# Kernel optimization log

Hardware: AMD Instinct MI355X
Metric: run time of the kernel (lower is better)

Reference implementation:

```python
import jax, jax.numpy as jnp
import numpy as np

N = 100_000   # nodes
E = 1_600_000 # edges
F = 128       # featurenum
H = 32        # hidden size (hard-coded in module)
G = 256       # graphs in batch


def setup_inputs() -> dict:
    key = jax.random.key(0)
    ks = jax.random.split(key, 10)
    x = jax.random.normal(ks[0], (N, F), jnp.float32)
    edge_index = jax.random.randint(ks[1], (2, E), 0, N)
    edge_attr = jax.random.randint(ks[2], (E, 1), 0, 4)
    batch = jnp.sort(jax.random.randint(ks[3], (N,), 0, G))
    def w(k, shape, fan):
        return jax.random.normal(k, shape, jnp.float32) / np.float32(np.sqrt(fan))
    W1 = w(ks[4], (F, H), F); b1 = jnp.zeros((H,), jnp.float32)
    W2 = w(ks[5], (H, H), H); b2 = jnp.zeros((H,), jnp.float32)
    Wl = w(ks[6], (H, 4 * H), H); bl = jnp.zeros((4 * H,), jnp.float32)
    Wm1 = w(ks[7], (H, H), H); bm1 = jnp.zeros((H,), jnp.float32)
    Wm2 = w(ks[8], (H, 1), H); bm2 = jnp.zeros((1,), jnp.float32)
    return dict(x=x, edge_index=edge_index, edge_attr=edge_attr, batch=batch,
                W1=W1, b1=b1, W2=W2, b2=b2, Wl=Wl, bl=bl,
                Wm1=Wm1, bm1=bm1, Wm2=Wm2, bm2=bm2)


def gcn_conv(x, src, tgt, W, b, n):
    # PyG GCNConv: add self-loops, symmetric normalization D^-1/2 (A+I) D^-1/2
    xw = x @ W                                            # [n, out]
    ones = jnp.ones(tgt.shape[0], x.dtype)
    deg = jax.ops.segment_sum(ones, tgt, num_segments=n) + 1.0  # in-degree + self-loop
    dinv = jax.lax.rsqrt(deg)
    msg = (dinv[src] * dinv[tgt])[:, None] * xw[src]      # [E, out]
    out = jax.ops.segment_sum(msg, tgt, num_segments=n)
    out = out + xw * (1.0 / deg)[:, None]                 # self-loop term (norm = 1/deg)
    return out + b


def reference(x, edge_index, edge_attr, batch, W1, b1, W2, b2, Wl, bl, Wm1, bm1, Wm2, bm2):
    n = x.shape[0]
    src, tgt = edge_index[0], edge_index[1]
    h = jax.nn.relu(gcn_conv(x, src, tgt, W1, b1, n))
    h = jax.nn.relu(gcn_conv(h, src, tgt, W2, b2, n))
    # MPNNl: linear -> (n, 4, H), gather slot per edge, scatter-mean to targets
    hl = (h @ Wl + bl).reshape(n, 4, H)
    rs = hl[src, edge_attr[:, 0]]                         # [E, H]
    cnt = jax.ops.segment_sum(jnp.ones(tgt.shape[0], h.dtype), tgt, num_segments=n)
    agg = jax.ops.segment_sum(rs, tgt, num_segments=n) / jnp.maximum(cnt, 1.0)[:, None]
    # global mean pool over graphs
    gcnt = jax.ops.segment_sum(jnp.ones(n, h.dtype), batch, num_segments=G)
    g = jax.ops.segment_sum(agg, batch, num_segments=G) / jnp.maximum(gcnt, 1.0)[:, None]
    # dropout in eval mode = identity; MLP + sigmoid
    out = jax.nn.relu(g @ Wm1 + bm1) @ Wm2 + bm2
    return jax.nn.sigmoid(out)                            # [G, 1]
```

## Files before the change

kernel.cpp:

```cpp
#include <hip/hip_runtime.h>
#include <hip/hip_bf16.h>
#include <stdint.h>

#define CDIV(a, b) (((a) + (b) - 1) / (b))

constexpr int BSH = 9;
#define TILE_A 2048

__global__ __launch_bounds__(256) void coarse_hist_k(const int* __restrict__ tgt,
                                                     int* __restrict__ bcnt, int E, int nb) {
    __shared__ int h[512];
    int t = threadIdx.x;
    for (int i = t; i < nb; i += 256) h[i] = 0;
    __syncthreads();
    for (int e = blockIdx.x * 256 + t; e < E; e += gridDim.x * 256)
        atomicAdd(&h[tgt[e] >> BSH], 1);
    __syncthreads();
    for (int i = t; i < nb; i += 256)
        if (h[i]) atomicAdd(&bcnt[i], h[i]);
}

__global__ __launch_bounds__(256) void bucket_scan_k(const int* __restrict__ bcnt,
                                                     int* __restrict__ bbase,
                                                     int* __restrict__ bcur, int nb, int E) {
    __shared__ int sp[256];
    int t = threadIdx.x;
    int c0 = (2 * t < nb) ? bcnt[2 * t] : 0;
    int c1 = (2 * t + 1 < nb) ? bcnt[2 * t + 1] : 0;
    int s2 = c0 + c1;
    sp[t] = s2;
    __syncthreads();
    for (int off = 1; off < 256; off <<= 1) {
        int x = (t >= off) ? sp[t - off] : 0;
        __syncthreads();
        sp[t] += x;
        __syncthreads();
    }
    int excl = sp[t] - s2;
    if (2 * t < nb) { bbase[2 * t] = excl; bcur[2 * t] = excl; }
    if (2 * t + 1 < nb) { bbase[2 * t + 1] = excl + c0; bcur[2 * t + 1] = excl + c0; }
    if (t == 0) bbase[nb] = E;
}

__global__ __launch_bounds__(256) void binA_k(const int* __restrict__ ei,
                                              const int* __restrict__ ea,
                                              int* __restrict__ bcur,
                                              unsigned long long* __restrict__ tmp, int E) {
    __shared__ unsigned long long stage[TILE_A];
    __shared__ int h_cnt[512], h_excl[512], h_cur[512], h_run[512], sp[256];
    int t = threadIdx.x;
    int base = blockIdx.x * TILE_A;
    int nt = min(TILE_A, E - base);
    for (int i = t; i < 512; i += 256) { h_cnt[i] = 0; h_cur[i] = 0; }
    __syncthreads();
    unsigned long long pk[8];
    int bk[8];
#pragma unroll
    for (int k = 0; k < 8; ++k) {
        int e = base + t + k * 256;
        bk[k] = -1;
        if (e < E) {
            int s = ei[e], tg = ei[E + e];
            unsigned a = (unsigned)ea[e];
            pk[k] = ((unsigned long long)(unsigned)tg << 20) |
                    ((unsigned long long)a << 18) | (unsigned long long)(unsigned)s;
            bk[k] = tg >> BSH;
            atomicAdd(&h_cnt[bk[k]], 1);
        }
    }
    __syncthreads();
    int c0 = h_cnt[2 * t], c1 = h_cnt[2 * t + 1];
    int s2 = c0 + c1;
    sp[t] = s2;
    __syncthreads();
    for (int off = 1; off < 256; off <<= 1) {
        int x = (t >= off) ? sp[t - off] : 0;
        __syncthreads();
        sp[t] += x;
        __syncthreads();
    }
    int excl = sp[t] - s2;
    h_excl[2 * t] = excl;
    h_excl[2 * t + 1] = excl + c0;
    __syncthreads();
    for (int i = t; i < 512; i += 256)
        if (h_cnt[i]) h_run[i] = atomicAdd(&bcur[i], h_cnt[i]);
#pragma unroll
    for (int k = 0; k < 8; ++k) {
        if (bk[k] >= 0) {
            int r = atomicAdd(&h_cur[bk[k]], 1);
            stage[h_excl[bk[k]] + r] = pk[k];
        }
    }
    __syncthreads();
    for (int i = t; i < nt; i += 256) {
        unsigned long long v = stage[i];
        int b = (int)(v >> 20) >> BSH;
        tmp[h_run[b] + (i - h_excl[b])] = v;
    }
}

__global__ __launch_bounds__(256) void binB_k(const unsigned long long* __restrict__ tmp,
                                              const int* __restrict__ bbase,
                                              unsigned* __restrict__ adj,
                                              int* __restrict__ rowptr4,
                                              float* __restrict__ dinv, int N, int E) {
    __shared__ int ncnt4[2048], nbase4[2048], ncur4[2048], sp[256];
    int t = threadIdx.x, b = blockIdx.x;
    int e0 = bbase[b], e1 = bbase[b + 1];
    int node0 = b << BSH;
    int nn = min(512, N - node0);
    for (int i = t; i < 2048; i += 256) { ncnt4[i] = 0; ncur4[i] = 0; }
    __syncthreads();
    for (int e = e0 + t; e < e1; e += 256) {
        unsigned long long v = tmp[e];
        int li = (int)(v >> 20) - node0;
        int q = (int)(v >> 18) & 3;
        atomicAdd(&ncnt4[li * 4 + q], 1);
    }
    __syncthreads();
    int loc[8];
    int s = 0;
#pragma unroll
    for (int k = 0; k < 8; ++k) { loc[k] = ncnt4[t * 8 + k]; s += loc[k]; }
    sp[t] = s;
    __syncthreads();
    for (int off = 1; off < 256; off <<= 1) {
        int x = (t >= off) ? sp[t - off] : 0;
        __syncthreads();
        sp[t] += x;
        __syncthreads();
    }
    int run = sp[t] - s;
#pragma unroll
    for (int k = 0; k < 8; ++k) { nbase4[t * 8 + k] = run; run += loc[k]; }
    __syncthreads();
    for (int i = t; i < nn; i += 256) {
        int node = node0 + i;
        *(int4*)&rowptr4[node * 4] = make_int4(e0 + nbase4[i * 4], e0 + nbase4[i * 4 + 1],
                                               e0 + nbase4[i * 4 + 2], e0 + nbase4[i * 4 + 3]);
        int c = ncnt4[i * 4] + ncnt4[i * 4 + 1] + ncnt4[i * 4 + 2] + ncnt4[i * 4 + 3];
        dinv[node] = rsqrtf((float)c + 1.0f);
    }
    if (b == 0 && t == 0) rowptr4[N * 4] = E;
    for (int e = e0 + t; e < e1; e += 256) {
        unsigned long long v = tmp[e];
        int li = (int)(v >> 20) - node0;
        int q = (int)(v >> 18) & 3;
        int r = atomicAdd(&ncur4[li * 4 + q], 1);
        adj[e0 + nbase4[li * 4 + q] + r] = (unsigned)(v & 0xFFFFFull);
    }
}

__device__ __forceinline__ int lb_sorted(const int* __restrict__ b, int n, int g) {
    int lo = 0, hi = n;
    while (lo < hi) {
        int m = (lo + hi) >> 1;
        if (b[m] < g) lo = m + 1; else hi = m;
    }
    return lo;
}

__global__ __launch_bounds__(256) void gbounds_k(const int* __restrict__ batch,
                                                 int* __restrict__ gcnt, int n, int Gn) {
    int g = blockIdx.x * 256 + threadIdx.x;
    if (g < Gn) {
        int a = lb_sorted(batch, n, g);
        int b2 = lb_sorted(batch, n, g + 1);
        gcnt[g] = b2 - a;
    }
}

__device__ __forceinline__ ushort f2bf(float v) {
    __hip_bfloat16 b = __float2bfloat16(v);
    return *reinterpret_cast<ushort*>(&b);
}
__device__ __forceinline__ float bflo(unsigned u) { return __uint_as_float(u << 16); }
__device__ __forceinline__ float bfhi(unsigned u) { return __uint_as_float(u & 0xFFFF0000u); }

template <int K, int COUT, int R, typename OutT>
__global__ __launch_bounds__(256) void gemm_rk(const float* __restrict__ X,
                                               const float* __restrict__ W,
                                               const float* __restrict__ bias,
                                               const float* __restrict__ dinv,
                                               OutT* __restrict__ Y, int nrows) {
    constexpr int NCG = COUT / 8;
    constexpr int RG = 256 / NCG;
    constexpr int ROWS = RG * R;
    constexpr int WS = K + 5;
    __shared__ float wt[COUT][WS];
    int t = threadIdx.x;
    for (int i = t; i < K * COUT; i += 256) {
        int k = i / COUT, j = i % COUT;
        wt[j][k] = W[i];
    }
    __syncthreads();
    int cg = t % NCG, g = t / NCG;
    int j0 = cg * 8;
    long rowbase = (long)blockIdx.x * ROWS + (long)g * R;
    float acc[R][8];
#pragma unroll
    for (int r = 0; r < R; ++r)
#pragma unroll
        for (int j = 0; j < 8; ++j) acc[r][j] = 0.0f;

    long rr[R];
#pragma unroll
    for (int r = 0; r < R; ++r) {
        long q = rowbase + r;
        rr[r] = (q < nrows) ? q : (long)(nrows - 1);
    }
    for (int k0 = 0; k0 < K; k0 += 4) {
        float4 xv[R];
#pragma unroll
        for (int r = 0; r < R; ++r) xv[r] = *(const float4*)(X + rr[r] * K + k0);
        float4 wv[8];
#pragma unroll
        for (int j = 0; j < 8; ++j) wv[j] = *(const float4*)&wt[j0 + j][k0];
#pragma unroll
        for (int r = 0; r < R; ++r)
#pragma unroll
            for (int j = 0; j < 8; ++j) {
                acc[r][j] += xv[r].x * wv[j].x;
                acc[r][j] += xv[r].y * wv[j].y;
                acc[r][j] += xv[r].z * wv[j].z;
                acc[r][j] += xv[r].w * wv[j].w;
            }
    }
#pragma unroll
    for (int r = 0; r < R; ++r) {
        long row = rowbase + r;
        if (row < nrows) {
            float dv = dinv ? dinv[row] : 1.0f;
            float o[8];
#pragma unroll
            for (int j = 0; j < 8; ++j) {
                float v = acc[r][j];
                if (bias) v += bias[j0 + j];
                o[j] = v * dv;
            }
            if constexpr (sizeof(OutT) == 4) {
                float4 o0 = make_float4(o[0], o[1], o[2], o[3]);
                float4 o1 = make_float4(o[4], o[5], o[6], o[7]);
                *(float4*)&Y[row * COUT + j0] = o0;
                *(float4*)&Y[row * COUT + j0 + 4] = o1;
            } else {
                uint4 u;
                u.x = (unsigned)f2bf(o[0]) | ((unsigned)f2bf(o[1]) << 16);
                u.y = (unsigned)f2bf(o[2]) | ((unsigned)f2bf(o[3]) << 16);
                u.z = (unsigned)f2bf(o[4]) | ((unsigned)f2bf(o[5]) << 16);
                u.w = (unsigned)f2bf(o[6]) | ((unsigned)f2bf(o[7]) << 16);
                *(uint4*)&Y[row * COUT + j0] = u;
            }
        }
    }
}


template <typename OutT>
__global__ __launch_bounds__(256) void agg_conv_k(const uint2* __restrict__ xwd4,
                                                  const unsigned* __restrict__ adj,
                                                  const int* __restrict__ rowptr4,
                                                  const float* __restrict__ dinv,
                                                  const float* __restrict__ bias,
                                                  OutT* __restrict__ out, int n) {
    int t = threadIdx.x;
    int node = blockIdx.x * 32 + (t >> 3);
    int f4 = t & 7;
    if (node >= n) return;
    int e0 = rowptr4[node * 4];
    int e1 = rowptr4[node * 4 + 4];
    float a0 = 0.f, a1 = 0.f, a2 = 0.f, a3 = 0.f;
    for (int e = e0; e < e1; e += 4) {
        int end1 = e1 - 1;
        int i1 = min(e + 1, end1), i2 = min(e + 2, end1), i3 = min(e + 3, end1);
        unsigned s0 = adj[e] & 0x3FFFF, s1 = adj[i1] & 0x3FFFF;
        unsigned s2 = adj[i2] & 0x3FFFF, s3 = adj[i3] & 0x3FFFF;
        uint2 u0 = xwd4[s0 * 8 + f4];
        uint2 u1 = xwd4[s1 * 8 + f4];
        uint2 u2 = xwd4[s2 * 8 + f4];
        uint2 u3 = xwd4[s3 * 8 + f4];
        bool v1 = e + 1 < e1, v2 = e + 2 < e1, v3 = e + 3 < e1;
        u1.x = v1 ? u1.x : 0u; u1.y = v1 ? u1.y : 0u;
        u2.x = v2 ? u2.x : 0u; u2.y = v2 ? u2.y : 0u;
        u3.x = v3 ? u3.x : 0u; u3.y = v3 ? u3.y : 0u;
        a0 += (bflo(u0.x) + bflo(u1.x)) + (bflo(u2.x) + bflo(u3.x));
        a1 += (bfhi(u0.x) + bfhi(u1.x)) + (bfhi(u2.x) + bfhi(u3.x));
        a2 += (bflo(u0.y) + bflo(u1.y)) + (bflo(u2.y) + bflo(u3.y));
        a3 += (bfhi(u0.y) + bfhi(u1.y)) + (bfhi(u2.y) + bfhi(u3.y));
    }
    float dvn = dinv[node];
    float degv = (float)(e1 - e0) + 1.0f;
    float sself = 1.0f / (dvn * degv);
    uint2 un = xwd4[node * 8 + f4];
    int c0i = 4 * f4;
    float v0 = fmaxf(dvn * a0 + bflo(un.x) * sself + bias[c0i], 0.0f);
    float v1 = fmaxf(dvn * a1 + bfhi(un.x) * sself + bias[c0i + 1], 0.0f);
    float v2 = fmaxf(dvn * a2 + bflo(un.y) * sself + bias[c0i + 2], 0.0f);
    float v3 = fmaxf(dvn * a3 + bfhi(un.y) * sself + bias[c0i + 3], 0.0f);
    if constexpr (sizeof(OutT) == 4) {
        *(float4*)&out[node * 32 + c0i] = make_float4(v0, v1, v2, v3);
    } else {
        uint2 w;
        w.x = (unsigned)f2bf(v0) | ((unsigned)f2bf(v1) << 16);
        w.y = (unsigned)f2bf(v2) | ((unsigned)f2bf(v3) << 16);
        ((uint2*)out)[node * 8 + f4] = w;
    }
}

#define RUN_ACC4(START, END, A)                                             \
    for (int e = (START); e < (END); e += 4) {                              \
        int end1 = (END) - 1;                                               \
        int i1 = min(e + 1, end1), i2 = min(e + 2, end1), i3 = min(e + 3, end1); \
        unsigned s0 = adj[e] & 0x3FFFF, s1 = adj[i1] & 0x3FFFF;             \
        unsigned s2 = adj[i2] & 0x3FFFF, s3 = adj[i3] & 0x3FFFF;            \
        uint2 u0 = h2q[s0 * 8 + f4];                                        \
        uint2 u1 = h2q[s1 * 8 + f4];                                        \
        uint2 u2 = h2q[s2 * 8 + f4];                                        \
        uint2 u3 = h2q[s3 * 8 + f4];                                        \
        bool v1 = e + 1 < (END), v2 = e + 2 < (END), v3 = e + 3 < (END);    \
        u1.x = v1 ? u1.x : 0u; u1.y = v1 ? u1.y : 0u;                       \
        u2.x = v2 ? u2.x : 0u; u2.y = v2 ? u2.y : 0u;                       \
        u3.x = v3 ? u3.x : 0u; u3.y = v3 ? u3.y : 0u;                       \
        (A).x += (bflo(u0.x) + bflo(u1.x)) + (bflo(u2.x) + bflo(u3.x));     \
        (A).y += (bfhi(u0.x) + bfhi(u1.x)) + (bfhi(u2.x) + bfhi(u3.x));     \
        (A).z += (bflo(u0.y) + bflo(u1.y)) + (bflo(u2.y) + bflo(u3.y));     \
        (A).w += (bfhi(u0.y) + bfhi(u1.y)) + (bfhi(u2.y) + bfhi(u3.y));     \
    }

__global__ __launch_bounds__(256) void agg_rs_fused_k(const uint2* __restrict__ h2q,
                                                      const unsigned* __restrict__ adj,
                                                      const int* __restrict__ rowptr4,
                                                      const float* __restrict__ Wl,
                                                      const float* __restrict__ bl,
                                                      float* __restrict__ out, int n) {
    constexpr int AS = 132;
    __shared__ float wls[32][128];
    __shared__ float bls[128];
    __shared__ float accs[32][AS];
    int t = threadIdx.x;
    for (int i = t; i < 4096; i += 256) wls[i >> 7][i & 127] = Wl[i];
    if (t < 128) bls[t] = bl[t];
    __syncthreads();

    int nl = t >> 3;
    int f4 = t & 7;
    int c0i = 4 * f4;
    int node = blockIdx.x * 32 + nl;
    if (node >= n) return;
    int4 rp = *(const int4*)&rowptr4[node * 4];
    int e4 = rowptr4[node * 4 + 4];
    float4 a0 = make_float4(0.f, 0.f, 0.f, 0.f);
    float4 a1 = a0, a2 = a0, a3 = a0;
    RUN_ACC4(rp.x, rp.y, a0)
    RUN_ACC4(rp.y, rp.z, a1)
    RUN_ACC4(rp.z, rp.w, a2)
    RUN_ACC4(rp.w, e4, a3)

    accs[nl][c0i] = a0.x;      accs[nl][c0i + 1] = a0.y;
    accs[nl][c0i + 2] = a0.z;  accs[nl][c0i + 3] = a0.w;
    accs[nl][32 + c0i] = a1.x;     accs[nl][32 + c0i + 1] = a1.y;
    accs[nl][32 + c0i + 2] = a1.z; accs[nl][32 + c0i + 3] = a1.w;
    accs[nl][64 + c0i] = a2.x;     accs[nl][64 + c0i + 1] = a2.y;
    accs[nl][64 + c0i + 2] = a2.z; accs[nl][64 + c0i + 3] = a2.w;
    accs[nl][96 + c0i] = a3.x;     accs[nl][96 + c0i + 1] = a3.y;
    accs[nl][96 + c0i + 2] = a3.z; accs[nl][96 + c0i + 3] = a3.w;
    float m0 = (float)(rp.y - rp.x), m1 = (float)(rp.z - rp.y);
    float m2 = (float)(rp.w - rp.z), m3 = (float)(e4 - rp.w);
    float o0 = m0 * bls[c0i] + m1 * bls[32 + c0i] + m2 * bls[64 + c0i] + m3 * bls[96 + c0i];
    float o1 = m0 * bls[c0i + 1] + m1 * bls[32 + c0i + 1] + m2 * bls[64 + c0i + 1] + m3 * bls[96 + c0i + 1];
    float o2 = m0 * bls[c0i + 2] + m1 * bls[32 + c0i + 2] + m2 * bls[64 + c0i + 2] + m3 * bls[96 + c0i + 2];
    float o3 = m0 * bls[c0i + 3] + m1 * bls[32 + c0i + 3] + m2 * bls[64 + c0i + 3] + m3 * bls[96 + c0i + 3];
#pragma unroll 8
    for (int j = 0; j < 32; ++j) {
        float q0 = accs[nl][j], q1 = accs[nl][32 + j];
        float q2 = accs[nl][64 + j], q3 = accs[nl][96 + j];
        float4 w0 = *(const float4*)&wls[j][c0i];
        float4 w1 = *(const float4*)&wls[j][32 + c0i];
        float4 w2 = *(const float4*)&wls[j][64 + c0i];
        float4 w3 = *(const float4*)&wls[j][96 + c0i];
        o0 += q0 * w0.x + q1 * w1.x + q2 * w2.x + q3 * w3.x;
        o1 += q0 * w0.y + q1 * w1.y + q2 * w2.y + q3 * w3.y;
        o2 += q0 * w0.z + q1 * w1.z + q2 * w2.z + q3 * w3.z;
        o3 += q0 * w0.w + q1 * w1.w + q2 * w2.w + q3 * w3.w;
    }
    float c = fmaxf((float)(e4 - rp.x), 1.0f);
    float ic = 1.0f / c;
    *(float4*)&out[node * 32 + c0i] = make_float4(o0 * ic, o1 * ic, o2 * ic, o3 * ic);
}


__global__ __launch_bounds__(256) void graph_sum_k(const float* __restrict__ agg,
                                                   const int* __restrict__ batch,
                                                   float* __restrict__ gsum, int n) {
    const int CHUNK = 128;
    int t = threadIdx.x;
    int f = t & 31;
    int j = t >> 5;
    long base = (long)blockIdx.x * (8 * CHUNK) + (long)j * CHUNK;
    if (base >= n) return;
    int end = (int)((n - base < CHUNK) ? (n - base) : CHUNK);
    int cur = batch[base];
    float acc = 0.0f;
    for (int i = 0; i < end; ++i) {
        int b = batch[base + i];
        if (b != cur) {
            atomicAdd(&gsum[cur * 32 + f], acc);
            acc = 0.0f;
            cur = b;
        }
        acc += agg[(base + i) * 32 + f];
    }
    atomicAdd(&gsum[cur * 32 + f], acc);
}


__global__ __launch_bounds__(256) void mlp_k(const float* __restrict__ gsum,
                                             const int* __restrict__ gcnt,
                                             const float* __restrict__ Wm1,
                                             const float* __restrict__ bm1,
                                             const float* __restrict__ Wm2,
                                             const float* __restrict__ bm2,
                                             float* __restrict__ out, int Gn) {
    __shared__ float w1[1024];
    __shared__ float w2[32];
    __shared__ float b1s[32];
    int t = threadIdx.x;
    for (int i = t; i < 1024; i += 256) w1[i] = Wm1[i];
    if (t < 32) {
        w2[t] = Wm2[t];
        b1s[t] = bm1[t];
    }
    __syncthreads();
    if (t < Gn) {
        float inv = 1.0f / fmaxf((float)gcnt[t], 1.0f);
        float gm[32];
#pragma unroll
        for (int k = 0; k < 32; ++k) gm[k] = gsum[t * 32 + k] * inv;
        float o = bm2[0];
        for (int j = 0; j < 32; ++j) {
            float h = b1s[j];
#pragma unroll
            for (int k = 0; k < 32; ++k) h += gm[k] * w1[k * 32 + j];
            o += fmaxf(h, 0.0f) * w2[j];
        }
        out[t] = 1.0f / (1.0f + expf(-o));
    }
}


extern "C" void kernel_launch(void* const* d_in, const int* in_sizes, int n_in,
                              void* d_out, int out_size, void* d_ws, size_t ws_size,
                              hipStream_t stream) {
    const float* x = (const float*)d_in[0];
    const int* ei = (const int*)d_in[1];
    const int* ea = (const int*)d_in[2];
    const int* batch = (const int*)d_in[3];
    const float* W1 = (const float*)d_in[4];
    const float* b1 = (const float*)d_in[5];
    const float* W2 = (const float*)d_in[6];
    const float* b2 = (const float*)d_in[7];
    const float* Wl = (const float*)d_in[8];
    const float* bl = (const float*)d_in[9];
    const float* Wm1 = (const float*)d_in[10];
    const float* bm1 = (const float*)d_in[11];
    const float* Wm2 = (const float*)d_in[12];
    const float* bm2 = (const float*)d_in[13];

    const int N = in_sizes[3];
    const int E = in_sizes[2];
    const int Gn = out_size;
    const int NBUCKET = CDIV(N, 512);

    char* ws = (char*)d_ws;
    size_t off = 0;
    auto alloc = [&](size_t bytes) -> void* {
        void* p = ws + off;
        off = (off + bytes + 255) & ~(size_t)255;
        return p;
    };
    int* rowptr4 = (int*)alloc((size_t)(4 * N + 4) * 4);
    float* dinv = (float*)alloc((size_t)N * 4);
    int* bcnt = (int*)alloc(512 * 4);
    int* bbase = (int*)alloc(513 * 4);
    int* bcur = (int*)alloc(512 * 4);
    unsigned* adj = (unsigned*)alloc((size_t)E * 4);
    float* gsum = (float*)alloc((size_t)Gn * 32 * 4);
    int* gcnt = (int*)alloc((size_t)Gn * 4);
    float* bufA = (float*)alloc((size_t)N * 32 * 4);
    float* bufB = (float*)alloc((size_t)N * 32 * 4);
    ushort* xw_bf = (ushort*)alloc((size_t)N * 32 * 2);
    ushort* h2bf = (ushort*)alloc((size_t)N * 32 * 2);
    unsigned long long* tmp = (unsigned long long*)alloc((size_t)E * 8);

    if (off > ws_size || NBUCKET > 512) return;

    hipMemsetAsync(bcnt, 0, 512 * 4, stream);
    hipMemsetAsync(gsum, 0, (size_t)Gn * 32 * 4, stream);

    coarse_hist_k<<<400, 256, 0, stream>>>(ei + E, bcnt, E, NBUCKET);
    bucket_scan_k<<<1, 256, 0, stream>>>(bcnt, bbase, bcur, NBUCKET, E);
    binA_k<<<CDIV(E, TILE_A), 256, 0, stream>>>(ei, ea, bcur, tmp, E);
    binB_k<<<NBUCKET, 256, 0, stream>>>(tmp, bbase, adj, rowptr4, dinv, N, E);
    gbounds_k<<<CDIV(Gn, 256), 256, 0, stream>>>(batch, gcnt, N, Gn);

    gemm_rk<128, 32, 1, ushort><<<CDIV(N, 64), 256, 0, stream>>>(x, W1, nullptr, dinv, xw_bf, N);
    agg_conv_k<float><<<CDIV(N, 32), 256, 0, stream>>>((const uint2*)xw_bf, adj, rowptr4,
                                                       dinv, b1, bufB, N);
    gemm_rk<32, 32, 1, ushort><<<CDIV(N, 64), 256, 0, stream>>>(bufB, W2, nullptr, dinv, xw_bf, N);
    agg_conv_k<ushort><<<CDIV(N, 32), 256, 0, stream>>>((const uint2*)xw_bf, adj, rowptr4,
                                                        dinv, b2, h2bf, N);
    agg_rs_fused_k<<<CDIV(N, 32), 256, 0, stream>>>((const uint2*)h2bf, adj, rowptr4,
                                                    Wl, bl, bufA, N);
    graph_sum_k<<<CDIV(N, 1024), 256, 0, stream>>>(bufA, batch, gsum, N);
    mlp_k<<<1, 256, 0, stream>>>(gsum, gcnt, Wm1, bm1, Wm2, bm2, (float*)d_out, Gn);
}
```

Before: 288.6 us.

## Sort nodes by in-degree to balance warp work in aggregation kernels

Adds a counting sort of nodes by in-degree (histogram, scan, scatter) that produces a permutation. The three aggregation kernels then process nodes in descending-degree order, so nodes of similar degree share a wavefront and divergence from uneven edge loops drops. In exchange it adds three small kernels plus an extra indirection per node, and output writes and input reads become scattered rather than sequential by node id. Atomic-based scatter makes the order within a degree class nondeterministic.

```diff
diff --git a/kernel.cpp b/kernel.cpp
--- a/kernel.cpp
+++ b/kernel.cpp
@@ -149,6 +149,53 @@
         int q = (int)(v >> 18) & 3;
         int r = atomicAdd(&ncur4[li * 4 + q], 1);
         adj[e0 + nbase4[li * 4 + q] + r] = (unsigned)(v & 0xFFFFFull);
+    }
+}
+
+__global__ __launch_bounds__(256) void dhist_k(const int* __restrict__ rowptr4,
+                                               int* __restrict__ dcnt, int N) {
+    __shared__ int h[512];
+    int t = threadIdx.x;
+    for (int i = t; i < 512; i += 256) h[i] = 0;
+    __syncthreads();
+    for (int node = blockIdx.x * 256 + t; node < N; node += gridDim.x * 256) {
+        int deg = min(rowptr4[node * 4 + 4] - rowptr4[node * 4], 511);
+        atomicAdd(&h[deg], 1);
+    }
+    __syncthreads();
+    for (int i = t; i < 512; i += 256)
+        if (h[i]) atomicAdd(&dcnt[i], h[i]);
+}
+
+__global__ __launch_bounds__(256) void dscan_k(const int* __restrict__ dcnt,
+                                               int* __restrict__ dbase,
+                                               int* __restrict__ dcur) {
+    __shared__ int sp[256];
+    int t = threadIdx.x;
+    int c0 = dcnt[511 - 2 * t];
+    int c1 = dcnt[511 - (2 * t + 1)];
+    int s2 = c0 + c1;
+    sp[t] = s2;
+    __syncthreads();
+    for (int off = 1; off < 256; off <<= 1) {
+        int x = (t >= off) ? sp[t - off] : 0;
+        __syncthreads();
+        sp[t] += x;
+        __syncthreads();
+    }
+    int excl = sp[t] - s2;
+    dbase[511 - 2 * t] = excl;       dcur[511 - 2 * t] = excl;
+    dbase[511 - 2 * t - 1] = excl + c0; dcur[511 - 2 * t - 1] = excl + c0;
+}
+
+__global__ __launch_bounds__(256) void dscatter_k(const int* __restrict__ rowptr4,
+                                                  int* __restrict__ dcur,
+                                                  int* __restrict__ perm, int N) {
+    int node = blockIdx.x * 256 + threadIdx.x;
+    if (node < N) {
+        int deg = min(rowptr4[node * 4 + 4] - rowptr4[node * 4], 511);
+        int pos = atomicAdd(&dcur[deg], 1);
+        perm[pos] = node;
     }
 }
 
@@ -261,13 +308,15 @@
 __global__ __launch_bounds__(256) void agg_conv_k(const uint2* __restrict__ xwd4,
                                                   const unsigned* __restrict__ adj,
                                                   const int* __restrict__ rowptr4,
+                                                  const int* __restrict__ perm,
                                                   const float* __restrict__ dinv,
                                                   const float* __restrict__ bias,
                                                   OutT* __restrict__ out, int n) {
     int t = threadIdx.x;
-    int node = blockIdx.x * 32 + (t >> 3);
+    int gi = blockIdx.x * 32 + (t >> 3);
     int f4 = t & 7;
-    if (node >= n) return;
+    if (gi >= n) return;
+    int node = perm[gi];
     int e0 = rowptr4[node * 4];
     int e1 = rowptr4[node * 4 + 4];
     float a0 = 0.f, a1 = 0.f, a2 = 0.f, a3 = 0.f;
@@ -331,6 +380,7 @@
 __global__ __launch_bounds__(256) void agg_rs_fused_k(const uint2* __restrict__ h2q,
                                                       const unsigned* __restrict__ adj,
                                                       const int* __restrict__ rowptr4,
+                                                      const int* __restrict__ perm,
                                                       const float* __restrict__ Wl,
                                                       const float* __restrict__ bl,
                                                       float* __restrict__ out, int n) {
@@ -346,8 +396,9 @@
     int nl = t >> 3;
     int f4 = t & 7;
     int c0i = 4 * f4;
-    int node = blockIdx.x * 32 + nl;
-    if (node >= n) return;
+    int gi = blockIdx.x * 32 + nl;
+    if (gi >= n) return;
+    int node = perm[gi];
     int4 rp = *(const int4*)&rowptr4[node * 4];
     int e4 = rowptr4[node * 4 + 4];
     float4 a0 = make_float4(0.f, 0.f, 0.f, 0.f);
@@ -482,8 +533,12 @@
     int* rowptr4 = (int*)alloc((size_t)(4 * N + 4) * 4);
     float* dinv = (float*)alloc((size_t)N * 4);
     int* bcnt = (int*)alloc(512 * 4);
+    int* dcnt = (int*)alloc(512 * 4);
     int* bbase = (int*)alloc(513 * 4);
     int* bcur = (int*)alloc(512 * 4);
+    int* dbase = (int*)alloc(512 * 4);
+    int* dcur = (int*)alloc(512 * 4);
+    int* perm = (int*)alloc((size_t)N * 4);
     unsigned* adj = (unsigned*)alloc((size_t)E * 4);
     float* gsum = (float*)alloc((size_t)Gn * 32 * 4);
     int* gcnt = (int*)alloc((size_t)Gn * 4);
@@ -495,23 +550,26 @@
 
     if (off > ws_size || NBUCKET > 512) return;
 
-    hipMemsetAsync(bcnt, 0, 512 * 4, stream);
+    hipMemsetAsync(bcnt, 0, 1024 * 4, stream);
     hipMemsetAsync(gsum, 0, (size_t)Gn * 32 * 4, stream);
 
     coarse_hist_k<<<400, 256, 0, stream>>>(ei + E, bcnt, E, NBUCKET);
     bucket_scan_k<<<1, 256, 0, stream>>>(bcnt, bbase, bcur, NBUCKET, E);
     binA_k<<<CDIV(E, TILE_A), 256, 0, stream>>>(ei, ea, bcur, tmp, E);
     binB_k<<<NBUCKET, 256, 0, stream>>>(tmp, bbase, adj, rowptr4, dinv, N, E);
+    dhist_k<<<400, 256, 0, stream>>>(rowptr4, dcnt, N);
+    dscan_k<<<1, 256, 0, stream>>>(dcnt, dbase, dcur);
+    dscatter_k<<<CDIV(N, 256), 256, 0, stream>>>(rowptr4, dcur, perm, N);
     gbounds_k<<<CDIV(Gn, 256), 256, 0, stream>>>(batch, gcnt, N, Gn);
 
     gemm_rk<128, 32, 1, ushort><<<CDIV(N, 64), 256, 0, stream>>>(x, W1, nullptr, dinv, xw_bf, N);
     agg_conv_k<float><<<CDIV(N, 32), 256, 0, stream>>>((const uint2*)xw_bf, adj, rowptr4,
-                                                       dinv, b1, bufB, N);
+                                                       perm, dinv, b1, bufB, N);
     gemm_rk<32, 32, 1, ushort><<<CDIV(N, 64), 256, 0, stream>>>(bufB, W2, nullptr, dinv, xw_bf, N);
     agg_conv_k<ushort><<<CDIV(N, 32), 256, 0, stream>>>((const uint2*)xw_bf, adj, rowptr4,
-                                                        dinv, b2, h2bf, N);
+                                                        perm, dinv, b2, h2bf, N);
     agg_rs_fused_k<<<CDIV(N, 32), 256, 0, stream>>>((const uint2*)h2bf, adj, rowptr4,
-                                                    Wl, bl, bufA, N);
+                                                    perm, Wl, bl, bufA, N);
     graph_sum_k<<<CDIV(N, 1024), 256, 0, stream>>>(bufA, batch, gsum, N);
     mlp_k<<<1, 256, 0, stream>>>(gsum, gcnt, Wm1, bm1, Wm2, bm2, (float*)d_out, Gn);
 }
```

Result: slower. 571.0 us (+97.9%).
